# Performance work log

Hardware: AMD Instinct MI355X
Metric: run time of the kernel (lower is better)

Reference implementation:

```python
import jax, jax.numpy as jnp
from jax import lax
import numpy as np

B, T, I, H, C = 32, 256, 128, 128, 100


def setup_inputs() -> dict:
    key = jax.random.key(0)
    ks = jax.random.split(key, 9)
    s = 1.0 / np.sqrt(H)  # PyTorch LSTMCell init range
    inp = {
        "x": jax.random.normal(ks[0], (B, T, I), dtype=jnp.float32),
        "w_ih": jax.random.uniform(ks[1], (4 * H, I), jnp.float32, -s, s),
        "b_ih": jax.random.uniform(ks[2], (4 * H,), jnp.float32, -s, s),
        "w_hh": jax.random.uniform(ks[3], (4 * H, H), jnp.float32, -s, s),
        "b_hh": jax.random.uniform(ks[4], (4 * H,), jnp.float32, -s, s),
        # attention params: normal(mean=0, std=0.01) per the source
        "w1": 0.01 * jax.random.normal(ks[5], (2 * H, H), dtype=jnp.float32),
        "w2": 0.01 * jax.random.normal(ks[6], (H, 1), dtype=jnp.float32),
        "w_fc": jax.random.uniform(ks[7], (C, H), jnp.float32, -s, s),
        "b_fc": jax.random.uniform(ks[8], (C,), jnp.float32, -s, s),
    }
    return inp


def _forward(x, w_ih, b_ih, w_hh, b_hh, w1, w2, w_fc, b_fc):
    Bv, Tv, _ = x.shape
    Hv = w_hh.shape[1]
    h0 = jnp.zeros((Bv, Hv), x.dtype)
    c0 = jnp.zeros((Bv, Hv), x.dtype)
    # memory buffer: slot 0 holds the initial zero hidden state (as in the
    # torch code, h_old starts as h_t=0); slots 1..T filled as we go.
    # Unwritten (future) slots are zero, so their attn contribution
    # attn_w * h_old is exactly zero -> no mask needed, matching the
    # growing-memory semantics of the original loop.
    mem0 = jnp.zeros((Bv, Tv + 1, Hv), x.dtype)
    attn0 = jnp.zeros((Bv, Hv), x.dtype)

    def step(carry, inp):
        h, c, mem, _ = carry
        x_t, i = inp
        # PyTorch LSTMCell: gate order i, f, g, o
        gates = x_t @ w_ih.T + b_ih + h @ w_hh.T + b_hh
        ig, fg, gg, og = jnp.split(gates, 4, axis=-1)
        c = jax.nn.sigmoid(fg) * c + jax.nn.sigmoid(ig) * jnp.tanh(gg)
        h = jax.nn.sigmoid(og) * jnp.tanh(c)
        # additive attention scores over the memory (NO softmax in source)
        h_rep = jnp.broadcast_to(h[:, None, :], mem.shape)  # [B, T+1, H]
        cat = jnp.concatenate([h_rep, mem], axis=-1)        # [B, T+1, 2H]
        s = jnp.tanh(cat @ w1) @ w2                          # [B, T+1, 1]
        attn_c = jnp.sum(s * mem, axis=1)                    # [B, H]
        mem = mem.at[:, i + 1, :].set(h)  # append h_t to memory
        return (h, c, mem, attn_c), None

    xs = (jnp.transpose(x, (1, 0, 2)), jnp.arange(Tv))
    (h, c, mem, attn_c), _ = lax.scan(step, (h0, c0, mem0, attn0), xs)
    return (h + attn_c) @ w_fc.T + b_fc


def reference(x, w_ih, b_ih, w_hh, b_hh, w1, w2, w_fc, b_fc):
    return _forward(x, w_ih, b_ih, w_hh, b_hh, w1, w2, w_fc, b_fc)
```

## Files before the change

### kernel.cpp

```cpp
#include <hip/hip_runtime.h>
#include <hip/hip_bf16.h>


#define Bsz 32
#define Tsz 256
#define Isz 128
#define Hsz 128
#define Csz 100
#define G4H 512

typedef short v8s __attribute__((ext_vector_type(8)));
typedef float v4fa __attribute__((ext_vector_type(4)));

__device__ __forceinline__ float2 pk_fma(float2 a, float2 b, float2 c) {
    float2 d;
    asm("v_pk_fma_f32 %0, %1, %2, %3" : "=v"(d) : "v"(a), "v"(b), "v"(c));
    return d;
}
__device__ __forceinline__ float quad_rsum(float x) {
    int t = __builtin_amdgcn_update_dpp(0, __float_as_int(x), 0xB1, 0xF, 0xF, true);
    x += __int_as_float(t);
    t = __builtin_amdgcn_update_dpp(0, __float_as_int(x), 0x4E, 0xF, 0xF, true);
    x += __int_as_float(t);
    return x;
}
__device__ __forceinline__ float oct_rsum(float x) {
    int t = __builtin_amdgcn_update_dpp(0, __float_as_int(x), 0xB1, 0xF, 0xF, true);
    x += __int_as_float(t);
    t = __builtin_amdgcn_update_dpp(0, __float_as_int(x), 0x4E, 0xF, 0xF, true);
    x += __int_as_float(t);
    t = __builtin_amdgcn_update_dpp(0, __float_as_int(x), 0x141, 0xF, 0xF, true);
    x += __int_as_float(t);
    return x;
}
__device__ __forceinline__ float rcpf(float x) { return __builtin_amdgcn_rcpf(x); }
__device__ __forceinline__ float ex2(float x) { return __builtin_amdgcn_exp2f(x); }
__device__ __forceinline__ float sigm_n(float x) {
    return rcpf(1.0f + ex2(-1.442695041f * x));
}
__device__ __forceinline__ float tanh_n(float x) {
    return fmaf(-2.0f, rcpf(1.0f + ex2(2.885390082f * x)), 1.0f);
}
__device__ __forceinline__ short bf16_bits(float x) {
    __hip_bfloat16 h = __float2bfloat16(x);
    return *reinterpret_cast<short*>(&h);
}
__device__ __forceinline__ float bf16_val(float x) {
    return __bfloat162float(__float2bfloat16(x));
}

__global__ __launch_bounds__(256) void prep_kernel(
    const float* __restrict__ w_ih, const float* __restrict__ b_ih,
    const float* __restrict__ w_hh, const float* __restrict__ b_hh,
    const float* __restrict__ w1,
    __hip_bfloat16* __restrict__ W2ih, __hip_bfloat16* __restrict__ W2v,
    float* __restrict__ whh_pk, float* __restrict__ bias) {
    int idx = blockIdx.x * blockDim.x + threadIdx.x;
    if (idx < G4H * Isz) {
        int n = idx >> 7;
        int k = idx & 127;
        float x = w_ih[idx];
        __hip_bfloat16 hi = __float2bfloat16(x);
        __hip_bfloat16 lo = __float2bfloat16(x - __bfloat162float(hi));
        W2ih[(size_t)n * 384 + k] = hi;
        W2ih[(size_t)n * 384 + 128 + k] = lo;
        W2ih[(size_t)n * 384 + 256 + k] = hi;

        int j4  = idx & 3;
        int q   = (idx >> 2) & 3;
        int d   = (idx >> 4) & 127;
        int gi  = (idx >> 11) & 3;
        int kk4 = (idx >> 13) & 7;
        whh_pk[idx] = w_hh[(size_t)((gi << 7) + d) * 128 + (q << 5) + (kk4 << 2) + j4];
    }
    if (idx < Hsz * Hsz) {
        int n = idx >> 7;
        int k = idx & 127;
        float x = w1[(size_t)(128 + k) * Hsz + n];
        __hip_bfloat16 hi = __float2bfloat16(x);
        __hip_bfloat16 lo = __float2bfloat16(x - __bfloat162float(hi));
        W2v[(size_t)n * 384 + k] = hi;
        W2v[(size_t)n * 384 + 128 + k] = lo;
        W2v[(size_t)n * 384 + 256 + k] = hi;
    }
    if (idx < G4H) bias[idx] = b_ih[idx] + b_hh[idx];
}

__global__ __launch_bounds__(256) void gemm_mfma_f32a(
    const float* __restrict__ A, const __hip_bfloat16* __restrict__ W2,
    const float* __restrict__ bias, float* __restrict__ C, int M, int N) {
    const int tid = threadIdx.x;
    const int w = tid >> 6, lane = tid & 63;
    const int m0 = blockIdx.y * 64 + (w & 1) * 32;
    const int n0 = blockIdx.x * 64 + (w >> 1) * 32;
    const int r = lane & 15, quad = lane >> 4;

    v8s Ahi[2][4], Alo[2][4];
    #pragma unroll
    for (int i = 0; i < 2; ++i)
        #pragma unroll
        for (int cb = 0; cb < 4; ++cb) {
            const float* src = A + (size_t)(m0 + 16 * i + r) * Isz + cb * 32 + quad * 8;
            float4 f0 = *(const float4*)src;
            float4 f1 = *(const float4*)(src + 4);
            float f[8] = {f0.x, f0.y, f0.z, f0.w, f1.x, f1.y, f1.z, f1.w};
            v8s hi, lo;
            #pragma unroll
            for (int e = 0; e < 8; ++e) {
                float hv = bf16_val(f[e]);
                hi[e] = bf16_bits(f[e]);
                lo[e] = bf16_bits(f[e] - hv);
            }
            Ahi[i][cb] = hi;
            Alo[i][cb] = lo;
        }

    v4fa acc[2][2] = {};
    const short* Wb = (const short*)W2;
    #pragma unroll
    for (int ks = 0; ks < 12; ++ks) {
        int cb = ks & 3;
        v8s a0 = (ks >= 8) ? Alo[0][cb] : Ahi[0][cb];
        v8s a1 = (ks >= 8) ? Alo[1][cb] : Ahi[1][cb];
        int kb = ks * 32 + quad * 8;
        v8s b0 = *(const v8s*)(Wb + (size_t)(n0 + r) * 384 + kb);
        v8s b1 = *(const v8s*)(Wb + (size_t)(n0 + 16 + r) * 384 + kb);
        acc[0][0] = __builtin_amdgcn_mfma_f32_16x16x32_bf16(a0, b0, acc[0][0], 0, 0, 0);
        acc[0][1] = __builtin_amdgcn_mfma_f32_16x16x32_bf16(a0, b1, acc[0][1], 0, 0, 0);
        acc[1][0] = __builtin_amdgcn_mfma_f32_16x16x32_bf16(a1, b0, acc[1][0], 0, 0, 0);
        acc[1][1] = __builtin_amdgcn_mfma_f32_16x16x32_bf16(a1, b1, acc[1][1], 0, 0, 0);
    }
    #pragma unroll
    for (int i = 0; i < 2; ++i)
        #pragma unroll
        for (int j = 0; j < 2; ++j) {
            int cn = n0 + 16 * j + r;
            float bb = bias ? bias[cn] : 0.0f;
            #pragma unroll
            for (int rr = 0; rr < 4; ++rr) {
                int row = m0 + 16 * i + quad * 4 + rr;
                C[(size_t)row * N + cn] = acc[i][j][rr] + bb;
            }
        }
}

#define HPAD(k) ((k) + 8 * ((k) >> 5))

__global__ __launch_bounds__(512, 2) void lstm_fused(
    const float* __restrict__ G, const float* __restrict__ whh_pk,
    const __hip_bfloat16* __restrict__ W2v,
    const float* __restrict__ w1, const float* __restrict__ w2,
    const float* __restrict__ w_fc, const float* __restrict__ b_fc,
    float* __restrict__ H_all, float* __restrict__ out) {
    const int b = blockIdx.x;
    const int tid = threadIdx.x;
    const int d = tid >> 2;
    const int q = tid & 3;

    __shared__ float h_s[2][160];
    __shared__ float kv_s[64][132];
    __shared__ float hT_s[Hsz];
    __shared__ float q_s[Hsz];
    __shared__ float w2s[Hsz];
    __shared__ float r_s[Hsz];
    __shared__ float s_s[64];
    __shared__ float part4[4][Hsz];

    float2 w2v[4][16];
    {
        const float4* wp = (const float4*)whh_pk;
        #pragma unroll
        for (int kk4 = 0; kk4 < 8; ++kk4)
            #pragma unroll
            for (int gi = 0; gi < 4; ++gi) {
                float4 v = wp[((kk4 * 4 + gi) * 128 + d) * 4 + q];
                w2v[gi][kk4 * 2]     = make_float2(v.x, v.y);
                w2v[gi][kk4 * 2 + 1] = make_float2(v.z, v.w);
            }
    }

    if (tid < 320) ((float*)h_s)[tid] = 0.0f;
    float c = 0.0f;
    __syncthreads();

    const float* Gq = G + (size_t)b * Tsz * G4H + q * 128 + d;
    float* Hst = H_all + (size_t)b * Tsz * Hsz + d;

    float gval = Gq[0];
    int cur = 0;
    for (int t = 0; t < Tsz; ++t) {
        const int tn = (t < Tsz - 1) ? t + 1 : t;
        float ngval = Gq[(size_t)tn * G4H];

        float2 accA[4], accB[4];
        #pragma unroll
        for (int gi = 0; gi < 4; ++gi) {
            accA[gi] = make_float2(q == gi ? gval : 0.f, 0.f);
            accB[gi] = make_float2(0.f, 0.f);
        }
        const float4* hb4 = (const float4*)&h_s[cur][q * 40];
        #pragma unroll
        for (int kk4 = 0; kk4 < 8; ++kk4) {
            float4 h4 = hb4[kk4];
            float2 hA = make_float2(h4.x, h4.y);
            float2 hB = make_float2(h4.z, h4.w);
            accA[0] = pk_fma(hA, w2v[0][2 * kk4], accA[0]);
            accA[1] = pk_fma(hA, w2v[1][2 * kk4], accA[1]);
            accA[2] = pk_fma(hA, w2v[2][2 * kk4], accA[2]);
            accA[3] = pk_fma(hA, w2v[3][2 * kk4], accA[3]);
            accB[0] = pk_fma(hB, w2v[0][2 * kk4 + 1], accB[0]);
            accB[1] = pk_fma(hB, w2v[1][2 * kk4 + 1], accB[1]);
            accB[2] = pk_fma(hB, w2v[2][2 * kk4 + 1], accB[2]);
            accB[3] = pk_fma(hB, w2v[3][2 * kk4 + 1], accB[3]);
        }
        float a0 = quad_rsum(accA[0].x + accA[0].y + accB[0].x + accB[0].y);
        float a1 = quad_rsum(accA[1].x + accA[1].y + accB[1].x + accB[1].y);
        float a2 = quad_rsum(accA[2].x + accA[2].y + accB[2].x + accB[2].y);
        float a3 = quad_rsum(accA[3].x + accA[3].y + accB[3].x + accB[3].y);

        float iv = sigm_n(a0);
        float fv = sigm_n(a1);
        float gv = tanh_n(a2);
        float ov = sigm_n(a3);
        c = fmaf(fv, c, iv * gv);
        float h = ov * tanh_n(c);

        if (q == 0) {
            h_s[cur ^ 1][HPAD(d)] = h;
            Hst[(size_t)t * Hsz] = h;
        }
        gval = ngval;
        __builtin_amdgcn_sched_barrier(0);
        asm volatile("s_waitcnt lgkmcnt(0)" ::: "memory");
        __builtin_amdgcn_s_barrier();
        __builtin_amdgcn_sched_barrier(0);
        cur ^= 1;
    }

    __syncthreads();

    const float* Hb = H_all + (size_t)b * Tsz * Hsz;
    const int n_a = tid >> 2;

    {
        if (tid < Hsz) {
            hT_s[tid] = h_s[cur][HPAD(tid)];
            w2s[tid] = w2[tid];
        }
        float acc = 0.f;
        #pragma unroll 8
        for (int kk = 0; kk < 32; ++kk) {
            int k = q * 32 + kk;
            acc = fmaf(h_s[cur][HPAD(k)], w1[(size_t)k * Hsz + n_a], acc);
        }
        acc = quad_rsum(acc);
        if (q == 0) q_s[n_a] = acc;
    }
    __syncthreads();

    const int w_id = tid >> 6;
    const int lane = tid & 63;
    const int fr = lane & 15, fq = lane >> 4;
    const int d_att = tid & 127, grp = tid >> 7;
    float racc = 0.f;

    for (int jt = 0; jt < 4; ++jt) {
        {
            const int m0 = (w_id & 1) * 32;
            const int n0 = (w_id >> 1) * 32;
            const float* Abase = Hb + (size_t)(jt * 64) * Hsz;

            v8s Ahi[2][4], Alo[2][4];
            #pragma unroll
            for (int i = 0; i < 2; ++i)
                #pragma unroll
                for (int cb = 0; cb < 4; ++cb) {
                    const float* src = Abase + (size_t)(m0 + 16 * i + fr) * Hsz + cb * 32 + fq * 8;
                    float4 f0 = *(const float4*)src;
                    float4 f1 = *(const float4*)(src + 4);
                    float f[8] = {f0.x, f0.y, f0.z, f0.w, f1.x, f1.y, f1.z, f1.w};
                    v8s hi, lo;
                    #pragma unroll
                    for (int e = 0; e < 8; ++e) {
                        float hv = bf16_val(f[e]);
                        hi[e] = bf16_bits(f[e]);
                        lo[e] = bf16_bits(f[e] - hv);
                    }
                    Ahi[i][cb] = hi;
                    Alo[i][cb] = lo;
                }

            v4fa a2[2][2] = {};
            const short* Wb = (const short*)W2v;
            #pragma unroll
            for (int ks = 0; ks < 12; ++ks) {
                int cb = ks & 3;
                v8s a0 = (ks >= 8) ? Alo[0][cb] : Ahi[0][cb];
                v8s a1 = (ks >= 8) ? Alo[1][cb] : Ahi[1][cb];
                int kb = ks * 32 + fq * 8;
                v8s b0 = *(const v8s*)(Wb + (size_t)(n0 + fr) * 384 + kb);
                v8s b1 = *(const v8s*)(Wb + (size_t)(n0 + 16 + fr) * 384 + kb);
                a2[0][0] = __builtin_amdgcn_mfma_f32_16x16x32_bf16(a0, b0, a2[0][0], 0, 0, 0);
                a2[0][1] = __builtin_amdgcn_mfma_f32_16x16x32_bf16(a0, b1, a2[0][1], 0, 0, 0);
                a2[1][0] = __builtin_amdgcn_mfma_f32_16x16x32_bf16(a1, b0, a2[1][0], 0, 0, 0);
                a2[1][1] = __builtin_amdgcn_mfma_f32_16x16x32_bf16(a1, b1, a2[1][1], 0, 0, 0);
            }
            #pragma unroll
            for (int i = 0; i < 2; ++i)
                #pragma unroll
                for (int j = 0; j < 2; ++j)
                    #pragma unroll
                    for (int rr = 0; rr < 4; ++rr)
                        kv_s[m0 + 16 * i + fq * 4 + rr][n0 + 16 * j + fr] = a2[i][j][rr];
        }
        __syncthreads();

        {
            const int jl = tid >> 3, oct = tid & 7;
            float p = 0.f;
            #pragma unroll
            for (int kk = 0; kk < 16; ++kk) {
                int k = oct * 16 + kk;
                p = fmaf(tanh_n(q_s[k] + kv_s[jl][k]), w2s[k], p);
            }
            p = oct_rsum(p);
            if (oct == 0) s_s[jl] = (jt * 64 + jl < 255) ? p : 0.0f;
        }
        __syncthreads();

        #pragma unroll 4
        for (int u = 0; u < 16; ++u) {
            int lj = grp * 16 + u;
            racc = fmaf(s_s[lj], Hb[(size_t)(jt * 64 + lj) * Hsz + d_att], racc);
        }
        __syncthreads();
    }

    part4[grp][d_att] = racc;
    __syncthreads();
    if (tid < Hsz)
        r_s[tid] = hT_s[tid] + part4[0][tid] + part4[1][tid] + part4[2][tid] + part4[3][tid];
    __syncthreads();

    {
        const int o = tid >> 2;
        float acc = 0.f;
        if (o < Csz) {
            #pragma unroll 8
            for (int kk = 0; kk < 32; ++kk) {
                int k = q * 32 + kk;
                acc = fmaf(r_s[k], w_fc[(size_t)o * Hsz + k], acc);
            }
        }
        acc = quad_rsum(acc);
        if (q == 0 && o < Csz) out[b * Csz + o] = acc + b_fc[o];
    }
}

extern "C" void kernel_launch(void* const* d_in, const int* in_sizes, int n_in,
                              void* d_out, int out_size, void* d_ws, size_t ws_size,
                              hipStream_t stream) {
    const float* x    = (const float*)d_in[0];
    const float* w_ih = (const float*)d_in[1];
    const float* b_ih = (const float*)d_in[2];
    const float* w_hh = (const float*)d_in[3];
    const float* b_hh = (const float*)d_in[4];
    const float* w1   = (const float*)d_in[5];
    const float* w2   = (const float*)d_in[6];
    const float* w_fc = (const float*)d_in[7];
    const float* b_fc = (const float*)d_in[8];

    float* ws = (float*)d_ws;
    float* whh_pk = ws;
    float* bias   = whh_pk + 65536;
    __hip_bfloat16* W2ih = (__hip_bfloat16*)(bias + 512);
    __hip_bfloat16* W2v  = (__hip_bfloat16*)(bias + 512 + 98304);
    float* G      = bias + 512 + 98304 + 24576;
    float* H_all  = G + 4194304;

    prep_kernel<<<256, 256, 0, stream>>>(w_ih, b_ih, w_hh, b_hh, w1,
                                         W2ih, W2v, whh_pk, bias);

    dim3 gG(G4H / 64, (Bsz * Tsz) / 64);
    gemm_mfma_f32a<<<gG, 256, 0, stream>>>(x, W2ih, bias, G, Bsz * Tsz, G4H);

    lstm_fused<<<Bsz, 512, 0, stream>>>(G, whh_pk, W2v, w1, w2, w_fc, b_fc,
                                        H_all, (float*)d_out);
}
```

Measured before the change: 311.8 us.

## Fuse input-projection GEMM into the LSTM kernel prologue per batch

Removes the separate MFMA GEMM launch that computed x·W_ih^T+bias for all batches. Each LSTM block now computes its own batch's gate preactivations with the same split-bf16 MFMA scheme before the recurrence, writes them to global G, syncs, then proceeds. This saves a kernel launch and inter-kernel gap. In exchange, the GEMM runs on only 32 blocks instead of spreading across the whole GPU, which serializes that work onto the recurrent critical path.

```diff
diff --git a/kernel.cpp b/kernel.cpp
--- a/kernel.cpp
+++ b/kernel.cpp
@@ -86,76 +86,24 @@
     if (idx < G4H) bias[idx] = b_ih[idx] + b_hh[idx];
 }
 
-__global__ __launch_bounds__(256) void gemm_mfma_f32a(
-    const float* __restrict__ A, const __hip_bfloat16* __restrict__ W2,
-    const float* __restrict__ bias, float* __restrict__ C, int M, int N) {
-    const int tid = threadIdx.x;
-    const int w = tid >> 6, lane = tid & 63;
-    const int m0 = blockIdx.y * 64 + (w & 1) * 32;
-    const int n0 = blockIdx.x * 64 + (w >> 1) * 32;
-    const int r = lane & 15, quad = lane >> 4;
-
-    v8s Ahi[2][4], Alo[2][4];
-    #pragma unroll
-    for (int i = 0; i < 2; ++i)
-        #pragma unroll
-        for (int cb = 0; cb < 4; ++cb) {
-            const float* src = A + (size_t)(m0 + 16 * i + r) * Isz + cb * 32 + quad * 8;
-            float4 f0 = *(const float4*)src;
-            float4 f1 = *(const float4*)(src + 4);
-            float f[8] = {f0.x, f0.y, f0.z, f0.w, f1.x, f1.y, f1.z, f1.w};
-            v8s hi, lo;
-            #pragma unroll
-            for (int e = 0; e < 8; ++e) {
-                float hv = bf16_val(f[e]);
-                hi[e] = bf16_bits(f[e]);
-                lo[e] = bf16_bits(f[e] - hv);
-            }
-            Ahi[i][cb] = hi;
-            Alo[i][cb] = lo;
-        }
-
-    v4fa acc[2][2] = {};
-    const short* Wb = (const short*)W2;
-    #pragma unroll
-    for (int ks = 0; ks < 12; ++ks) {
-        int cb = ks & 3;
-        v8s a0 = (ks >= 8) ? Alo[0][cb] : Ahi[0][cb];
-        v8s a1 = (ks >= 8) ? Alo[1][cb] : Ahi[1][cb];
-        int kb = ks * 32 + quad * 8;
-        v8s b0 = *(const v8s*)(Wb + (size_t)(n0 + r) * 384 + kb);
-        v8s b1 = *(const v8s*)(Wb + (size_t)(n0 + 16 + r) * 384 + kb);
-        acc[0][0] = __builtin_amdgcn_mfma_f32_16x16x32_bf16(a0, b0, acc[0][0], 0, 0, 0);
-        acc[0][1] = __builtin_amdgcn_mfma_f32_16x16x32_bf16(a0, b1, acc[0][1], 0, 0, 0);
-        acc[1][0] = __builtin_amdgcn_mfma_f32_16x16x32_bf16(a1, b0, acc[1][0], 0, 0, 0);
-        acc[1][1] = __builtin_amdgcn_mfma_f32_16x16x32_bf16(a1, b1, acc[1][1], 0, 0, 0);
-    }
-    #pragma unroll
-    for (int i = 0; i < 2; ++i)
-        #pragma unroll
-        for (int j = 0; j < 2; ++j) {
-            int cn = n0 + 16 * j + r;
-            float bb = bias ? bias[cn] : 0.0f;
-            #pragma unroll
-            for (int rr = 0; rr < 4; ++rr) {
-                int row = m0 + 16 * i + quad * 4 + rr;
-                C[(size_t)row * N + cn] = acc[i][j][rr] + bb;
-            }
-        }
-}
-
 #define HPAD(k) ((k) + 8 * ((k) >> 5))
 
 __global__ __launch_bounds__(512, 2) void lstm_fused(
-    const float* __restrict__ G, const float* __restrict__ whh_pk,
+    const float* __restrict__ x, const __hip_bfloat16* __restrict__ W2ih,
+    const float* __restrict__ bias,
+    const float* __restrict__ whh_pk,
     const __hip_bfloat16* __restrict__ W2v,
     const float* __restrict__ w1, const float* __restrict__ w2,
     const float* __restrict__ w_fc, const float* __restrict__ b_fc,
-    float* __restrict__ H_all, float* __restrict__ out) {
+    float* __restrict__ G, float* __restrict__ H_all,
+    float* __restrict__ out) {
     const int b = blockIdx.x;
     const int tid = threadIdx.x;
     const int d = tid >> 2;
     const int q = tid & 3;
+    const int w_id = tid >> 6;
+    const int lane = tid & 63;
+    const int fr = lane & 15, fq = lane >> 4;
 
     __shared__ float h_s[2][160];
     __shared__ float kv_s[64][132];
@@ -166,6 +114,65 @@
     __shared__ float s_s[64];
     __shared__ float part4[4][Hsz];
 
+    float* Gb = G + (size_t)b * Tsz * G4H;
+
+    {
+        const float* Ab = x + (size_t)b * Tsz * Isz;
+        const int m0 = w_id * 32;
+
+        v8s Ahi[2][4], Alo[2][4];
+        #pragma unroll
+        for (int i = 0; i < 2; ++i)
+            #pragma unroll
+            for (int cb = 0; cb < 4; ++cb) {
+                const float* src = Ab + (size_t)(m0 + 16 * i + fr) * Isz + cb * 32 + fq * 8;
+                float4 f0 = *(const float4*)src;
+                float4 f1 = *(const float4*)(src + 4);
+                float f[8] = {f0.x, f0.y, f0.z, f0.w, f1.x, f1.y, f1.z, f1.w};
+                v8s hi, lo;
+                #pragma unroll
+                for (int e = 0; e < 8; ++e) {
+                    float hv = bf16_val(f[e]);
+                    hi[e] = bf16_bits(f[e]);
+                    lo[e] = bf16_bits(f[e] - hv);
+                }
+                Ahi[i][cb] = hi;
+                Alo[i][cb] = lo;
+            }
+
+        const short* Wb = (const short*)W2ih;
+        for (int nt = 0; nt < 16; ++nt) {
+            const int n0 = nt * 32;
+            v4fa acc[2][2] = {};
+            #pragma unroll
+            for (int ks = 0; ks < 12; ++ks) {
+                int cb = ks & 3;
+                v8s a0 = (ks >= 8) ? Alo[0][cb] : Ahi[0][cb];
+                v8s a1 = (ks >= 8) ? Alo[1][cb] : Ahi[1][cb];
+                int kb = ks * 32 + fq * 8;
+                v8s b0 = *(const v8s*)(Wb + (size_t)(n0 + fr) * 384 + kb);
+                v8s b1 = *(const v8s*)(Wb + (size_t)(n0 + 16 + fr) * 384 + kb);
+                acc[0][0] = __builtin_amdgcn_mfma_f32_16x16x32_bf16(a0, b0, acc[0][0], 0, 0, 0);
+                acc[0][1] = __builtin_amdgcn_mfma_f32_16x16x32_bf16(a0, b1, acc[0][1], 0, 0, 0);
+                acc[1][0] = __builtin_amdgcn_mfma_f32_16x16x32_bf16(a1, b0, acc[1][0], 0, 0, 0);
+                acc[1][1] = __builtin_amdgcn_mfma_f32_16x16x32_bf16(a1, b1, acc[1][1], 0, 0, 0);
+            }
+            #pragma unroll
+            for (int i = 0; i < 2; ++i)
+                #pragma unroll
+                for (int j = 0; j < 2; ++j) {
+                    int cn = n0 + 16 * j + fr;
+                    float bb = bias[cn];
+                    #pragma unroll
+                    for (int rr = 0; rr < 4; ++rr) {
+                        int row = m0 + 16 * i + fq * 4 + rr;
+                        Gb[(size_t)row * G4H + cn] = acc[i][j][rr] + bb;
+                    }
+                }
+        }
+    }
+    __syncthreads();
+
     float2 w2v[4][16];
     {
         const float4* wp = (const float4*)whh_pk;
@@ -183,7 +190,7 @@
     float c = 0.0f;
     __syncthreads();
 
-    const float* Gq = G + (size_t)b * Tsz * G4H + q * 128 + d;
+    const float* Gq = Gb + q * 128 + d;
     float* Hst = H_all + (size_t)b * Tsz * Hsz + d;
 
     float gval = Gq[0];
@@ -258,9 +265,6 @@
     }
     __syncthreads();
 
-    const int w_id = tid >> 6;
-    const int lane = tid & 63;
-    const int fr = lane & 15, fq = lane >> 4;
     const int d_att = tid & 127, grp = tid >> 7;
     float racc = 0.f;
 
@@ -381,9 +385,7 @@
     prep_kernel<<<256, 256, 0, stream>>>(w_ih, b_ih, w_hh, b_hh, w1,
                                          W2ih, W2v, whh_pk, bias);
 
-    dim3 gG(G4H / 64, (Bsz * Tsz) / 64);
-    gemm_mfma_f32a<<<gG, 256, 0, stream>>>(x, W2ih, bias, G, Bsz * Tsz, G4H);
-
-    lstm_fused<<<Bsz, 512, 0, stream>>>(G, whh_pk, W2v, w1, w2, w_fc, b_fc,
-                                        H_all, (float*)d_out);
-}
+    lstm_fused<<<Bsz, 512, 0, stream>>>(x, W2ih, bias, whh_pk, W2v,
+                                        w1, w2, w_fc, b_fc,
+                                        G, H_all, (float*)d_out);
+}
```

New measurement: 386.6 us. 24.0% more time.
